# Optimization experiments

Hardware: AMD Instinct MI355X
Metric: run time of the kernel (lower is better)

## Reference

```python
import jax, jax.numpy as jnp
import numpy as np

E4M3 = jnp.float8_e4m3fn  # HPU e4m3 (max 240) approximated by e4m3fn grid
E5M2 = jnp.float8_e5m2


def fp8_quant_dequant(x, scale, dt):
    # cast_to_fp8(x, scale) followed by inline dequant (1/scale) inside fp8_gemm_v2
    return (x * scale).astype(dt).astype(jnp.float32) / scale


def setup_inputs() -> dict:
    key = jax.random.key(0)
    k1, k2 = jax.random.split(key)
    A, B, C, OUT = 4, 2048, 2048, 8192
    return {
        "input": jax.random.normal(k1, (A, B, C), jnp.float32),
        "weight": jax.random.normal(k2, (OUT, C), jnp.float32) * 0.02,
        "input_scale_e4m3": jnp.ones((), jnp.float32),
        "weight_scale_e4m3": jnp.ones((), jnp.float32),
        "input_scale_e5m2": jnp.ones((), jnp.float32),
        "weight_scale_e5m2": jnp.ones((), jnp.float32),
        "grad_scale_e5m2": jnp.ones((), jnp.float32),
    }


def reference(input, weight, input_scale_e4m3, weight_scale_e4m3,
              input_scale_e5m2, weight_scale_e5m2, grad_scale_e5m2):
    A, B, C = input.shape
    x2d = input.reshape(A * B, C)
    # forward path uses the e4m3 copies from cast_to_fp8_hybrid
    x_q = fp8_quant_dequant(x2d, input_scale_e4m3, E4M3)      # [A*B, C]
    w_q = fp8_quant_dequant(weight, weight_scale_e4m3, E4M3)  # [OUT, C]
    out = x_q @ w_q.T                                          # [A*B, OUT]
    return out.reshape(A, B, -1)
```

## Files before the change

kernel.cpp:

```cpp
#include <hip/hip_runtime.h>

typedef float floatx16 __attribute__((ext_vector_type(16)));
typedef int   intx4    __attribute__((ext_vector_type(4)));
typedef int   intx8    __attribute__((ext_vector_type(8)));

#define GEMM_M 8192
#define GEMM_N 8192
#define GEMM_K 2048
#define NT     32

__global__ __launch_bounds__(256) void quant_e4m3(const float* __restrict__ x,
                                                  const float* __restrict__ scale,
                                                  int* __restrict__ q)
{
    const float s = scale[0];
    const int base = blockIdx.x * 1024 + threadIdx.x;
    const float4* __restrict__ x4 = (const float4*)x;
#pragma unroll
    for (int j = 0; j < 4; ++j) {
        float4 v = x4[base + j * 256];
        int p;
        p = __builtin_amdgcn_cvt_pk_fp8_f32(v.x * s, v.y * s, 0, false);
        p = __builtin_amdgcn_cvt_pk_fp8_f32(v.z * s, v.w * s, p, true);
        q[base + j * 256] = p;
    }
}

#define GLDS(gp, lp) __builtin_amdgcn_global_load_lds( \
    (const __attribute__((address_space(1))) void*)(gp), \
    (__attribute__((address_space(3))) void*)(lp), 16, 0, 0)

__global__ __launch_bounds__(512, 2) void gemm_fp8_mx(
    const unsigned char* __restrict__ Aq,
    const unsigned char* __restrict__ Bq,
    float* __restrict__ C,
    const float* __restrict__ sa,
    const float* __restrict__ sb)
{
    extern __shared__ __align__(16) unsigned char lds[];
    unsigned char* ldsA = lds;
    unsigned char* ldsB = lds + 65536;

    const int tid  = threadIdx.x;
    const int lane = tid & 63;
    const int wave = tid >> 6;
    const int wm   = wave >> 2;
    const int wn   = wave & 3;

    const int bid = blockIdx.x;
    const int nb  = (bid & 7) * 128 + (bid >> 3);
    const int bm  = nb >> 5;
    const int bn  = nb & 31;

    const int srow   = tid >> 2;
    const int schunk = ((tid & 3) ^ ((tid >> 3) & 3)) << 4;
    const unsigned char* gA0 = Aq + (size_t)(bm * 256 +       srow) * GEMM_K + schunk;
    const unsigned char* gA1 = Aq + (size_t)(bm * 256 + 128 + srow) * GEMM_K + schunk;
    const unsigned char* gB0 = Bq + (size_t)(bn * 256 +       srow) * GEMM_K + schunk;
    const unsigned char* gB1 = Bq + (size_t)(bn * 256 + 128 + srow) * GEMM_K + schunk;
    const int l0 = tid * 16;

    const int mloc = lane & 31;
    const int h    = lane >> 5;
    const int swz  = (mloc >> 1) & 3;
    const int aoff_lo = (wm * 128 + mloc) * 64 + (((2 * h)     ^ swz) << 4);
    const int aoff_hi = (wm * 128 + mloc) * 64 + (((2 * h + 1) ^ swz) << 4);
    const int boff_lo = (wn * 64  + mloc) * 64 + (((2 * h)     ^ swz) << 4);
    const int boff_hi = (wn * 64  + mloc) * 64 + (((2 * h + 1) ^ swz) << 4);

    floatx16 acc[4][2];
#pragma unroll
    for (int i = 0; i < 4; ++i)
#pragma unroll
        for (int j = 0; j < 2; ++j)
            acc[i][j] = (floatx16)(0.0f);

#define STAGE(KT) do { \
    const int _b = (KT) & 3; \
    const size_t _ko = (size_t)(KT) * 64; \
    GLDS(gA0 + _ko, ldsA + _b * 16384 +        l0); \
    GLDS(gA1 + _ko, ldsA + _b * 16384 + 8192 + l0); \
    GLDS(gB0 + _ko, ldsB + _b * 16384 +        l0); \
    GLDS(gB1 + _ko, ldsB + _b * 16384 + 8192 + l0); \
} while (0)

#define KSTEP(KT, STAGE_STMT) do { \
    const unsigned char* _bA = ldsA + ((KT) & 3) * 16384; \
    const unsigned char* _bB = ldsB + ((KT) & 3) * 16384; \
    intx8 _a[4], _bf[2]; \
    _Pragma("unroll") \
    for (int _t = 0; _t < 4; ++_t) { \
        intx4 lo = *(const intx4*)(_bA + aoff_lo + _t * 2048); \
        intx4 hi = *(const intx4*)(_bA + aoff_hi + _t * 2048); \
        _a[_t] = __builtin_shufflevector(lo, hi, 0, 1, 2, 3, 4, 5, 6, 7); \
    } \
    _Pragma("unroll") \
    for (int _t = 0; _t < 2; ++_t) { \
        intx4 lo = *(const intx4*)(_bB + boff_lo + _t * 2048); \
        intx4 hi = *(const intx4*)(_bB + boff_hi + _t * 2048); \
        _bf[_t] = __builtin_shufflevector(lo, hi, 0, 1, 2, 3, 4, 5, 6, 7); \
    } \
    STAGE_STMT; \
    __builtin_amdgcn_s_setprio(1); \
    _Pragma("unroll") \
    for (int _i = 0; _i < 4; ++_i) \
    _Pragma("unroll") \
    for (int _j = 0; _j < 2; ++_j) \
        acc[_i][_j] = __builtin_amdgcn_mfma_scale_f32_32x32x64_f8f6f4( \
            _a[_i], _bf[_j], acc[_i][_j], \
            0, 0, 0, 0x7f7f7f7f, 0, 0x7f7f7f7f); \
    __builtin_amdgcn_s_setprio(0); \
} while (0)

#define BARRIER() do { asm volatile("" ::: "memory"); \
    __builtin_amdgcn_s_barrier(); \
    asm volatile("" ::: "memory"); } while (0)

    STAGE(0); STAGE(1); STAGE(2);
    asm volatile("s_waitcnt vmcnt(8)" ::: "memory");
    BARRIER();

#pragma unroll 1
    for (int kt = 0; kt <= NT - 4; ++kt) {
        KSTEP(kt, STAGE(kt + 3));
        asm volatile("s_waitcnt vmcnt(8)" ::: "memory");
        BARRIER();
    }
    KSTEP(NT - 3, (void)0);
    asm volatile("s_waitcnt vmcnt(4)" ::: "memory");
    BARRIER();
    KSTEP(NT - 2, (void)0);
    asm volatile("s_waitcnt vmcnt(0)" ::: "memory");
    BARRIER();
    KSTEP(NT - 1, (void)0);

    const float inv = 1.0f / (sa[0] * sb[0]);
#pragma unroll
    for (int ti = 0; ti < 4; ++ti) {
        const int row0 = bm * 256 + wm * 128 + ti * 32 + 4 * h;
#pragma unroll
        for (int tj = 0; tj < 2; ++tj) {
            const int col = bn * 256 + wn * 64 + tj * 32 + mloc;
#pragma unroll
            for (int reg = 0; reg < 16; ++reg) {
                const int row = row0 + (reg & 3) + 8 * (reg >> 2);
                C[(size_t)row * GEMM_N + col] = acc[ti][tj][reg] * inv;
            }
        }
    }
}

extern "C" void kernel_launch(void* const* d_in, const int* in_sizes, int n_in,
                              void* d_out, int out_size, void* d_ws, size_t ws_size,
                              hipStream_t stream) {
    const float* x    = (const float*)d_in[0];
    const float* w    = (const float*)d_in[1];
    const float* s_in = (const float*)d_in[2];
    const float* s_w  = (const float*)d_in[3];
    float* out = (float*)d_out;

    unsigned char* qx = (unsigned char*)d_ws;
    unsigned char* qw = qx + (size_t)GEMM_M * GEMM_K;

    quant_e4m3<<<in_sizes[0] / 4096, 256, 0, stream>>>(x, s_in, (int*)qx);
    quant_e4m3<<<in_sizes[1] / 4096, 256, 0, stream>>>(w, s_w, (int*)qw);

    static int attr_done = 0;
    if (!attr_done) {
        hipFuncSetAttribute((const void*)gemm_fp8_mx,
                            hipFuncAttributeMaxDynamicSharedMemorySize, 131072);
        attr_done = 1;
    }
    gemm_fp8_mx<<<dim3(1024), dim3(512), 131072, stream>>>(qx, qw, out, s_in, s_w);
}
```

Baseline: 487.4 us.

## Split each k-step into two barrier-synchronized phases and remap tiles per XCD

Each k-step is split into two phases, each loading half the A fragments (with B loaded once) and issuing four MFMAs. The phases are separated by extra s_barrier calls so that waves stay in lockstep and interleave LDS reads, global-to-LDS staging and MFMA work, similar to a ping-pong schedule. Fragment register use drops from six intx8 to four. The block-to-tile mapping now gives each XCD a 4-row band of M tiles traversed in 4x4 groups, aiming at better L2 reuse. In exchange there are twice as many barriers per k-step, and the forced lgkmcnt(0) waits may serialize LDS reads with MFMAs.

```diff
diff --git a/kernel.cpp b/kernel.cpp
--- a/kernel.cpp
+++ b/kernel.cpp
@@ -30,6 +30,9 @@
     (const __attribute__((address_space(1))) void*)(gp), \
     (__attribute__((address_space(3))) void*)(lp), 16, 0, 0)
 
+#define MFMA1(A_, B_, C_) __builtin_amdgcn_mfma_scale_f32_32x32x64_f8f6f4( \
+    (A_), (B_), (C_), 0, 0, 0, 0x7f7f7f7f, 0, 0x7f7f7f7f)
+
 __global__ __launch_bounds__(512, 2) void gemm_fp8_mx(
     const unsigned char* __restrict__ Aq,
     const unsigned char* __restrict__ Bq,
@@ -48,9 +51,10 @@
     const int wn   = wave & 3;
 
     const int bid = blockIdx.x;
-    const int nb  = (bid & 7) * 128 + (bid >> 3);
-    const int bm  = nb >> 5;
-    const int bn  = nb & 31;
+    const int xcd = bid & 7;
+    const int idx = bid >> 3;
+    const int bm  = xcd * 4 + ((idx & 15) >> 2);
+    const int bn  = (idx >> 4) * 4 + (idx & 3);
 
     const int srow   = tid >> 2;
     const int schunk = ((tid & 3) ^ ((tid >> 3) & 3)) << 4;
@@ -75,64 +79,80 @@
         for (int j = 0; j < 2; ++j)
             acc[i][j] = (floatx16)(0.0f);
 
-#define STAGE(KT) do { \
-    const int _b = (KT) & 3; \
-    const size_t _ko = (size_t)(KT) * 64; \
+    intx8 af0, af1, bf0, bf1;
+
+#define LDFRAG(dst, base, olo, ohi) do { \
+    intx4 _lo = *(const intx4*)((base) + (olo)); \
+    intx4 _hi = *(const intx4*)((base) + (ohi)); \
+    (dst) = __builtin_shufflevector(_lo, _hi, 0, 1, 2, 3, 4, 5, 6, 7); \
+} while (0)
+
+#define STAGE_A(KT) do { \
+    const int _b = (KT) & 3; const size_t _ko = (size_t)(KT) * 64; \
     GLDS(gA0 + _ko, ldsA + _b * 16384 +        l0); \
     GLDS(gA1 + _ko, ldsA + _b * 16384 + 8192 + l0); \
+} while (0)
+
+#define STAGE_B(KT) do { \
+    const int _b = (KT) & 3; const size_t _ko = (size_t)(KT) * 64; \
     GLDS(gB0 + _ko, ldsB + _b * 16384 +        l0); \
     GLDS(gB1 + _ko, ldsB + _b * 16384 + 8192 + l0); \
 } while (0)
 
-#define KSTEP(KT, STAGE_STMT) do { \
+#define P0(KT, STAGE_STMT) do { \
     const unsigned char* _bA = ldsA + ((KT) & 3) * 16384; \
     const unsigned char* _bB = ldsB + ((KT) & 3) * 16384; \
-    intx8 _a[4], _bf[2]; \
-    _Pragma("unroll") \
-    for (int _t = 0; _t < 4; ++_t) { \
-        intx4 lo = *(const intx4*)(_bA + aoff_lo + _t * 2048); \
-        intx4 hi = *(const intx4*)(_bA + aoff_hi + _t * 2048); \
-        _a[_t] = __builtin_shufflevector(lo, hi, 0, 1, 2, 3, 4, 5, 6, 7); \
-    } \
-    _Pragma("unroll") \
-    for (int _t = 0; _t < 2; ++_t) { \
-        intx4 lo = *(const intx4*)(_bB + boff_lo + _t * 2048); \
-        intx4 hi = *(const intx4*)(_bB + boff_hi + _t * 2048); \
-        _bf[_t] = __builtin_shufflevector(lo, hi, 0, 1, 2, 3, 4, 5, 6, 7); \
-    } \
+    LDFRAG(af0, _bA, aoff_lo,        aoff_hi); \
+    LDFRAG(af1, _bA, aoff_lo + 2048, aoff_hi + 2048); \
+    LDFRAG(bf0, _bB, boff_lo,        boff_hi); \
+    LDFRAG(bf1, _bB, boff_lo + 2048, boff_hi + 2048); \
     STAGE_STMT; \
+    __builtin_amdgcn_s_barrier(); \
+    asm volatile("s_waitcnt lgkmcnt(0)" ::: "memory"); \
     __builtin_amdgcn_s_setprio(1); \
-    _Pragma("unroll") \
-    for (int _i = 0; _i < 4; ++_i) \
-    _Pragma("unroll") \
-    for (int _j = 0; _j < 2; ++_j) \
-        acc[_i][_j] = __builtin_amdgcn_mfma_scale_f32_32x32x64_f8f6f4( \
-            _a[_i], _bf[_j], acc[_i][_j], \
-            0, 0, 0, 0x7f7f7f7f, 0, 0x7f7f7f7f); \
+    acc[0][0] = MFMA1(af0, bf0, acc[0][0]); \
+    acc[0][1] = MFMA1(af0, bf1, acc[0][1]); \
+    acc[1][0] = MFMA1(af1, bf0, acc[1][0]); \
+    acc[1][1] = MFMA1(af1, bf1, acc[1][1]); \
     __builtin_amdgcn_s_setprio(0); \
+    __builtin_amdgcn_s_barrier(); \
 } while (0)
 
-#define BARRIER() do { asm volatile("" ::: "memory"); \
+#define P1(KT, STAGE_STMT, TAILWAIT) do { \
+    const unsigned char* _bA = ldsA + ((KT) & 3) * 16384; \
+    LDFRAG(af0, _bA, aoff_lo + 4096, aoff_hi + 4096); \
+    LDFRAG(af1, _bA, aoff_lo + 6144, aoff_hi + 6144); \
+    STAGE_STMT; \
     __builtin_amdgcn_s_barrier(); \
-    asm volatile("" ::: "memory"); } while (0)
+    asm volatile("s_waitcnt lgkmcnt(0)" ::: "memory"); \
+    __builtin_amdgcn_s_setprio(1); \
+    acc[2][0] = MFMA1(af0, bf0, acc[2][0]); \
+    acc[2][1] = MFMA1(af0, bf1, acc[2][1]); \
+    acc[3][0] = MFMA1(af1, bf0, acc[3][0]); \
+    acc[3][1] = MFMA1(af1, bf1, acc[3][1]); \
+    __builtin_amdgcn_s_setprio(0); \
+    TAILWAIT; \
+    __builtin_amdgcn_s_barrier(); \
+} while (0)
 
-    STAGE(0); STAGE(1); STAGE(2);
+    STAGE_A(0); STAGE_B(0);
+    STAGE_A(1); STAGE_B(1);
+    STAGE_A(2); STAGE_B(2);
     asm volatile("s_waitcnt vmcnt(8)" ::: "memory");
-    BARRIER();
+    __builtin_amdgcn_s_barrier();
 
 #pragma unroll 1
     for (int kt = 0; kt <= NT - 4; ++kt) {
-        KSTEP(kt, STAGE(kt + 3));
-        asm volatile("s_waitcnt vmcnt(8)" ::: "memory");
-        BARRIER();
+        P0(kt, STAGE_A(kt + 3));
+        P1(kt, STAGE_B(kt + 3),
+           asm volatile("s_waitcnt vmcnt(8)" ::: "memory"));
     }
-    KSTEP(NT - 3, (void)0);
-    asm volatile("s_waitcnt vmcnt(4)" ::: "memory");
-    BARRIER();
-    KSTEP(NT - 2, (void)0);
-    asm volatile("s_waitcnt vmcnt(0)" ::: "memory");
-    BARRIER();
-    KSTEP(NT - 1, (void)0);
+    P0(NT - 3, (void)0);
+    P1(NT - 3, (void)0, asm volatile("s_waitcnt vmcnt(4)" ::: "memory"));
+    P0(NT - 2, (void)0);
+    P1(NT - 2, (void)0, asm volatile("s_waitcnt vmcnt(0)" ::: "memory"));
+    P0(NT - 1, (void)0);
+    P1(NT - 1, (void)0, (void)0);
 
     const float inv = 1.0f / (sa[0] * sb[0]);
 #pragma unroll
```

New measurement: 478.2 us. No clear change (-1.9%).
